# Optimization experiments

Hardware: AMD Instinct MI355X
Metric: run time of the kernel (lower is better)

The kernel has to match this reference:

```python
import jax, jax.numpy as jnp
import numpy as np

HEAD = 32  # HEAD_SIZE
B, T, C = 8, 1024, 768
LAYER_ID, N_LAYER = 2, 12


def wkv7(r, w, k, v, a, b):
    # RWKV7 linear recurrence (matches the custom CUDA 'attn' kernel math):
    #   S = S * exp(-exp(w)) + (S @ a) b^T + v k^T ;  y = S @ r
    Bb, Tt, Cc = r.shape
    H, N = Cc // HEAD, HEAD
    rs = lambda z: jnp.moveaxis(z.reshape(Bb, Tt, H, N), 1, 0)  # [T,B,H,N]
    rT, kT, vT, aT, bT = rs(r), rs(k), rs(v), rs(a), rs(b)
    wT = rs(jnp.exp(-jnp.exp(w)))  # decay in (0,1)
    def step(S, inp):
        rt, wt, kt, vt, at, bt = inp  # each [B,H,N]
        sa = jnp.einsum('bhij,bhj->bhi', S, at)
        S = S * wt[:, :, None, :] + sa[..., None] * bt[:, :, None, :] + vt[..., None] * kt[:, :, None, :]
        return S, jnp.einsum('bhij,bhj->bhi', S, rt)
    S0 = jnp.zeros((Bb, H, N, N), r.dtype)
    _, y = jax.lax.scan(step, S0, (rT, wT, kT, vT, aT, bT))
    return jnp.moveaxis(y, 0, 1).reshape(Bb, Tt, Cc)


def setup_inputs() -> dict:
    key = jax.random.key(0)
    ks = iter(jax.random.split(key, 64))
    def rn(shape, s=0.02):
        return (jax.random.normal(next(ks), shape, jnp.float32) * s)
    def un(shape, lim):
        return jax.random.uniform(next(ks), shape, jnp.float32, -lim, lim)
    H, N = C // HEAD, HEAD
    r10 = 1.0 - LAYER_ID / N_LAYER          # ratio_1_to_almost0
    r01 = LAYER_ID / (N_LAYER - 1)          # ratio_0_to_1
    ddd = (np.arange(C, dtype=np.float64) / C).reshape(1, 1, C)
    f32 = lambda z: jnp.asarray(z, jnp.float32)
    time_maa_x = f32(1.0 - ddd ** (0.6 * r10 ** 0.9))
    time_maa_rg = f32(1.0 - ddd ** (0.2 * r10))
    time_maa_wa = f32(1.0 - ddd ** (0.9 * r10))
    time_maa_k = f32(1.0 - (ddd ** (0.9 * r10) + 0.4 * r01))
    time_maa_v = f32(1.0 - (ddd ** (0.4 * r10) + 0.6 * r01))
    ds = -7.0 + 5.0 * (np.arange(C, dtype=np.float64) / (C - 1)) ** (0.85 + r01 ** 0.5)
    time_decay = f32(ds.reshape(1, 1, C) + 0.5)
    inp = {
        'x': jax.random.normal(next(ks), (B, T, C), jnp.float32),
        'v1': jax.random.normal(next(ks), (B, T, C), jnp.float32),
        'time_maa_x': time_maa_x, 'time_maa_rg': time_maa_rg, 'time_maa_wa': time_maa_wa,
        'time_maa_k': time_maa_k, 'time_maa_v': time_maa_v,
        'time_decay': time_decay,
        'time_faaaa': rn((1, 1, H, N), 0.05),
        'time_aaaaa': rn((1, 1, C), 0.05),
        'time_maa_w1': rn((C, 28 * 4)), 'time_maa_w2': rn((4, 28, C), 0.05),
        'time_decay_w1': rn((C, 64)), 'time_decay_w2': rn((64, C), 0.05),
        'time_aaa_w1': rn((C, 24)), 'time_aaa_w2': rn((24, C), 0.05),
        'time_kkk_w1': rn((C, 24)), 'time_kkk_w2': rn((24, C), 0.05),
        'gate_w1': rn((C, 120)), 'gate_w2': rn((120, C), 0.05),
        'ma_w1': rn((C, 24)), 'ma_w2': rn((24, C), 0.05), 'time_misc_a': rn((1, 1, C), 0.05),
        'mk_w1': rn((C, 24)), 'mk_w2': rn((24, C), 0.05), 'time_misc_k': rn((1, 1, C), 0.05),
        'mv_w1': rn((C, 24)), 'mv_w2': rn((24, C), 0.05), 'time_misc_v': 1.0 + rn((1, 1, C), 0.05),
        'Wr': un((C, C), 0.5 / C ** 0.5), 'Wk': un((C, C), 0.05 / C ** 0.5),
        'Wv': un((C, C), 0.5 / C ** 0.5), 'Wo': rn((C, C), 0.02),
        'ln_w': jnp.ones((C,), jnp.float32), 'ln_b': jnp.zeros((C,), jnp.float32),
    }
    return inp


def reference(x, v1, time_maa_x, time_maa_rg, time_maa_wa, time_maa_k, time_maa_v,
              time_decay, time_faaaa, time_aaaaa, time_maa_w1, time_maa_w2,
              time_decay_w1, time_decay_w2, time_aaa_w1, time_aaa_w2,
              time_kkk_w1, time_kkk_w2, gate_w1, gate_w2, ma_w1, ma_w2, time_misc_a,
              mk_w1, mk_w2, time_misc_k, mv_w1, mv_w2, time_misc_v,
              Wr, Wk, Wv, Wo, ln_w, ln_b):
    Bb, Tt, Cc = x.shape
    H, N = Cc // HEAD, HEAD
    # token shift: xx[t] = x[t-1] - x[t], with x[-1] = 0
    xsh = jnp.concatenate([jnp.zeros_like(x[:, :1]), x[:, :-1]], axis=1)
    xx = xsh - x
    xxx = x + xx * time_maa_x
    tm = jnp.tanh(xxx @ time_maa_w1).reshape(Bb, Tt, 4, -1)      # [B,T,4,28]
    mix = jnp.einsum('btfd,fdc->fbtc', tm, time_maa_w2)          # [4,B,T,C]
    xrg = x + xx * (time_maa_rg + mix[0])
    xwa = x + xx * (time_maa_wa + mix[1])
    xk = x + xx * (time_maa_k + mix[2])
    xv = x + xx * (time_maa_v + mix[3])
    r = xrg @ Wr
    w = -jax.nn.softplus(-(time_decay + jnp.tanh(xwa @ time_decay_w1) @ time_decay_w2)) - 0.5
    k = xk @ Wk
    v = xv @ Wv
    v = v + (v1 - v) * jax.nn.sigmoid(time_misc_v + xv @ mv_w1 @ mv_w2)
    g = jax.nn.sigmoid(xrg @ gate_w1) @ gate_w2
    kk = k + jnp.tanh(xk @ time_kkk_w1) @ time_kkk_w2
    kk4 = kk.reshape(Bb, Tt, H, N)
    nrm = jnp.maximum(jnp.sqrt(jnp.sum(kk4 * kk4, axis=-1, keepdims=True)), 1e-12)
    kk = (kk4 / nrm).reshape(Bb, Tt, Cc)
    a = jax.nn.sigmoid(time_aaaaa + xwa @ time_aaa_w1 @ time_aaa_w2)
    ma = jax.nn.sigmoid(time_misc_a + xwa @ ma_w1 @ ma_w2)
    k = k * ma + k * a * (1.0 - ma)
    mk = jax.nn.sigmoid(time_misc_k + xk @ mk_w1 @ mk_w2)
    k = k * jnp.exp(jnp.minimum(w * mk, 0.0))
    y = wkv7(r, w, k, v, -kk, kk * a)
    # GroupNorm(n_head groups) over each token, eps=6.4e-5
    yg = y.reshape(Bb, Tt, H, N)
    mu = jnp.mean(yg, axis=-1, keepdims=True)
    var = jnp.var(yg, axis=-1, keepdims=True)
    yn = (yg - mu) * jax.lax.rsqrt(var + 6.4e-05)
    yn = yn * ln_w.reshape(H, N) + ln_b.reshape(H, N)
    # per-head bonus term
    bonus = (jnp.sum(r.reshape(Bb, Tt, H, N) * k.reshape(Bb, Tt, H, N) * time_faaaa,
                     axis=-1, keepdims=True) * v.reshape(Bb, Tt, H, N))
    y = yn.reshape(Bb, Tt, Cc) + bonus.reshape(Bb, Tt, Cc)
    out = (y * g) @ Wo
    return (out, v1)
```

## Files before the change

kernel.cpp:

```cpp
#include <hip/hip_runtime.h>
#include <hip/hip_bf16.h>
#include <math.h>

#define Bdim 8
#define Tdim 1024
#define Cdim 768
#define Hdim 24
#define Ndim 32
#define BTdim (Bdim*Tdim)

typedef __attribute__((ext_vector_type(8))) short bf16x8;
typedef __attribute__((ext_vector_type(4))) float f32x4;
typedef __hip_bfloat16 bf16;

__device__ __forceinline__ float sigm(float x){ return 1.f/(1.f+expf(-x)); }
__device__ __forceinline__ float softplusf(float x){ return fmaxf(x,0.f) + log1pf(expf(-fabsf(x))); }
__device__ __forceinline__ float bf2f(bf16 v){ return __bfloat162float(v); }
__device__ __forceinline__ float us2f(unsigned short s){ return __builtin_bit_cast(float, (unsigned)s<<16); }

template<int CTRL>
__device__ __forceinline__ float dpp_add(float x){
  int xi = __builtin_bit_cast(int, x);
  int yi = __builtin_amdgcn_mov_dpp(xi, CTRL, 0xF, 0xF, true);
  return x + __builtin_bit_cast(float, yi);
}
__device__ __forceinline__ float red32(float x){
  x = dpp_add<0xB1>(x);
  x = dpp_add<0x4E>(x);
  x = dpp_add<0x141>(x);
  x = dpp_add<0x140>(x);
  x += __shfl_xor(x, 16);
  return x;
}
__device__ __forceinline__ float red16(float x){
  x = dpp_add<0xB1>(x);
  x = dpp_add<0x4E>(x);
  x = dpp_add<0x141>(x);
  x = dpp_add<0x140>(x);
  return x;
}

#define GLDS16(gp, lp) __builtin_amdgcn_global_load_lds((const __attribute__((address_space(1))) void*)(gp), (__attribute__((address_space(3))) void*)(lp), 16, 0, 0)

__global__ void k1_shift(const float* __restrict__ x, const float* __restrict__ maa_x,
                         bf16* __restrict__ xxx) {
  int idx = blockIdx.x*256 + threadIdx.x;
  if (idx >= BTdim*Cdim) return;
  int c = idx % Cdim; int row = idx / Cdim; int t = row % Tdim;
  float xv = x[idx];
  float xp = (t==0) ? 0.f : x[idx - Cdim];
  xxx[idx] = __float2bfloat16(xv + (xp - xv)*maa_x[c]);
}

__global__ __launch_bounds__(256) void kcp(const float* __restrict__ W0, const float* __restrict__ W1,
    const float* __restrict__ W2, const float* __restrict__ W3,
    bf16* __restrict__ T0, bf16* __restrict__ T1, bf16* __restrict__ T2, bf16* __restrict__ T3,
    const float* __restrict__ dw1, const float* __restrict__ aaa_w1,
    const float* __restrict__ ma_w1, const float* __restrict__ kkk_w1, const float* __restrict__ mk_w1,
    const float* __restrict__ mv_w1, const float* __restrict__ gate_w1, const float* __restrict__ maa_w1,
    const float* __restrict__ dw2, const float* __restrict__ aaa_w2, const float* __restrict__ ma_w2,
    const float* __restrict__ kkk_w2, const float* __restrict__ mk_w2, const float* __restrict__ mv_w2,
    const float* __restrict__ gate_w2,
    bf16* __restrict__ PWwa, bf16* __restrict__ PWk, bf16* __restrict__ PWv,
    bf16* __restrict__ PWrg, bf16* __restrict__ PWmaa,
    bf16* __restrict__ W2wa, bf16* __restrict__ W2k, bf16* __restrict__ W2v, bf16* __restrict__ W2g){
  const int bid = blockIdx.x;
  if (bid < 2304) {
    __shared__ float tile[32][33];
    const int z = bid/576, rem = bid - z*576;
    const int by = (rem/24)*32, bx = (rem%24)*32;
    const float* Wsrc[4] = {W0,W1,W2,W3};
    bf16* Tdst[4] = {T0,T1,T2,T3};
    const float* W = Wsrc[z];
    bf16* T = Tdst[z];
    int tx = threadIdx.x & 31, ty = threadIdx.x >> 5;
    #pragma unroll
    for (int q=0;q<32;q+=8) tile[ty+q][tx] = W[(size_t)(by+ty+q)*Cdim + bx+tx];
    __syncthreads();
    #pragma unroll
    for (int q=0;q<32;q+=8) T[(size_t)(bx+ty+q)*Cdim + by+tx] = __float2bfloat16(tile[tx][ty+q]);
    return;
  }
  int idx = (bid-2304)*256 + threadIdx.x;
  if (idx < 491520) {
    int buf = idx / 98304, rem = idx - buf*98304;
    int n = rem / 768, kk = rem - n*768;
    float val = 0.f;
    bf16* dst;
    switch(buf){
      case 0: dst=PWwa; if(n<64) val=dw1[(size_t)kk*64+n]; else if(n<88) val=aaa_w1[(size_t)kk*24+(n-64)]; else if(n<112) val=ma_w1[(size_t)kk*24+(n-88)]; break;
      case 1: dst=PWk;  if(n<24) val=kkk_w1[(size_t)kk*24+n]; else if(n<48) val=mk_w1[(size_t)kk*24+(n-24)]; break;
      case 2: dst=PWv;  if(n<24) val=mv_w1[(size_t)kk*24+n]; break;
      case 3: dst=PWrg; if(n<120) val=gate_w1[(size_t)kk*120+n]; break;
      default: dst=PWmaa; if(n<112) val=maa_w1[(size_t)kk*112+n]; break;
    }
    dst[rem] = __float2bfloat16(val);
    return;
  }
  int i = idx - 491520;
  if (i < 294912){
    int n=i>>7, q=i&127, seg=n/768, c=n-seg*768;
    float val=0.f;
    if (seg==0){ if(q<64) val=dw2[(size_t)q*768+c]; }
    else if (seg==1){ if(q>=64&&q<88) val=aaa_w2[(size_t)(q-64)*768+c]; }
    else { if(q>=88&&q<112) val=ma_w2[(size_t)(q-88)*768+c]; }
    W2wa[i]=__float2bfloat16(val); return;
  }
  i -= 294912;
  if (i < 98304){
    int n=i>>6, q=i&63, seg=n/768, c=n-seg*768;
    float val=0.f;
    if (seg==0){ if(q<24) val=kkk_w2[(size_t)q*768+c]; }
    else { if(q>=24&&q<48) val=mk_w2[(size_t)(q-24)*768+c]; }
    W2k[i]=__float2bfloat16(val); return;
  }
  i -= 98304;
  if (i < 24576){
    int c=i>>5, q=i&31;
    float val = (q<24) ? mv_w2[(size_t)q*768+c] : 0.f;
    W2v[i]=__float2bfloat16(val); return;
  }
  i -= 24576;
  if (i < 98304){
    int c=i>>7, q=i&127;
    float val = (q<120) ? gate_w2[(size_t)q*768+c] : 0.f;
    W2g[i]=__float2bfloat16(val);
  }
}

__global__ __launch_bounds__(256) void gemm_wo(const bf16* __restrict__ A,
    const bf16* __restrict__ Bt, float* __restrict__ C, int N, int K) {
  __shared__ unsigned short As[64*32];
  __shared__ unsigned short Bs[128*32];
  const int bm = blockIdx.y*64, bn = blockIdx.x*128;
  const int tid = threadIdx.x, lane = tid&63, w = tid>>6;
  const int wr = w>>1, wc = w&1;
  const int lr = lane&15, kg = lane>>4;
  f32x4 zero = {0.f,0.f,0.f,0.f};
  f32x4 acc[2][4];
  #pragma unroll
  for (int m=0;m<2;m++)
    #pragma unroll
    for (int n=0;n<4;n++) acc[m][n]=zero;
  const size_t rowA = (size_t)(bm + w*16 + (lane>>2))*K + (lane&3)*8;
  const size_t rowB = (size_t)(bn + w*32 + (lane>>2))*K + (lane&3)*8;
  unsigned short* lA = As + w*16*32;
  unsigned short* lB = Bs + w*32*32;
  for (int k0=0; k0<K; k0+=32){
    GLDS16(A + rowA + k0,                 lA);
    GLDS16(Bt + rowB + k0,                lB);
    GLDS16(Bt + rowB + k0 + (size_t)16*K, lB + 512);
    __syncthreads();
    bf16x8 af[2], bfr[4];
    #pragma unroll
    for (int m=0;m<2;m++) af[m]  = *(const bf16x8*)(void*)(As + (wr*32+m*16+lr)*32 + kg*8);
    #pragma unroll
    for (int n=0;n<4;n++) bfr[n] = *(const bf16x8*)(void*)(Bs + (wc*64+n*16+lr)*32 + kg*8);
    #pragma unroll
    for (int m=0;m<2;m++)
      #pragma unroll
      for (int n=0;n<4;n++)
        acc[m][n] = __builtin_amdgcn_mfma_f32_16x16x32_bf16(af[m], bfr[n], acc[m][n], 0,0,0);
    __syncthreads();
  }
  #pragma unroll
  for (int m=0;m<2;m++)
    #pragma unroll
    for (int n=0;n<4;n++){
      size_t r0 = (size_t)(bm + wr*32 + m*16 + kg*4);
      int cc = bn + wc*64 + n*16 + lr;
      #pragma unroll
      for (int q=0;q<4;q++)
        C[(r0+q)*N + cc] = acc[m][n][q];
    }
}

__global__ __launch_bounds__(256) void gemm_tm(const bf16* __restrict__ A,
    const bf16* __restrict__ Bt, float* __restrict__ C, int K) {
  __shared__ unsigned short As[128*32];
  __shared__ unsigned short Bs[128*32];
  const int bm = blockIdx.y*128;
  const int tid = threadIdx.x, lane = tid&63, w = tid>>6;
  const int wr = w>>1, wc = w&1;
  const int lr = lane&15, kg = lane>>4;
  f32x4 zero = {0.f,0.f,0.f,0.f};
  f32x4 acc[4][4];
  #pragma unroll
  for (int m=0;m<4;m++)
    #pragma unroll
    for (int n=0;n<4;n++) acc[m][n]=zero;
  const size_t rowA = (size_t)(bm + w*32 + (lane>>2))*K + (lane&3)*8;
  const size_t rowB = (size_t)(w*32 + (lane>>2))*K + (lane&3)*8;
  unsigned short* lA = As + w*32*32;
  unsigned short* lB = Bs + w*32*32;
  for (int k0=0; k0<K; k0+=32){
    GLDS16(A + rowA + k0,                 lA);
    GLDS16(A + rowA + k0 + (size_t)16*K,  lA + 512);
    GLDS16(Bt + rowB + k0,                lB);
    GLDS16(Bt + rowB + k0 + (size_t)16*K, lB + 512);
    __syncthreads();
    bf16x8 af[4], bfr[4];
    #pragma unroll
    for (int m=0;m<4;m++) af[m]  = *(const bf16x8*)(void*)(As + (wr*64+m*16+lr)*32 + kg*8);
    #pragma unroll
    for (int n=0;n<4;n++) bfr[n] = *(const bf16x8*)(void*)(Bs + (wc*64+n*16+lr)*32 + kg*8);
    #pragma unroll
    for (int m=0;m<4;m++)
      #pragma unroll
      for (int n=0;n<4;n++)
        acc[m][n] = __builtin_amdgcn_mfma_f32_16x16x32_bf16(af[m], bfr[n], acc[m][n], 0,0,0);
    __syncthreads();
  }
  #pragma unroll
  for (int m=0;m<4;m++)
    #pragma unroll
    for (int n=0;n<4;n++){
      size_t r0 = (size_t)(bm + wr*64 + m*16 + kg*4);
      int cc = wc*64 + n*16 + lr;
      if (cc < 112){
        #pragma unroll
        for (int q=0;q<4;q++)
          C[(r0+q)*112 + cc] = tanhf(acc[m][n][q]);
      }
    }
}

struct S1P {
  const bf16* A[4];
  const bf16* Bt[4];
  bf16* C[4];
  int Ntrue[4];
  int Nalloc[4];
  int act[4];
};
struct G3 {
  const bf16* A[3];
  const bf16* Bt[3];
  bf16* C[3];
};
__global__ __launch_bounds__(256) void gemm_s1b3(S1P s, G3 g, int K) {
  const int bid = blockIdx.x;
  __shared__ unsigned short As[128*32];
  __shared__ unsigned short Bs[128*32];
  const int tid = threadIdx.x, lane = tid&63, w = tid>>6;
  const int wr = w>>1, wc = w&1;
  const int lr = lane&15, kg = lane>>4;
  int bm, bn, z;
  const bf16 *A, *Bt;
  const bool small = (bid < 256);
  if (small){
    z = bid>>6; bm = (bid&63)*128; bn = 0;
    A = s.A[z]; Bt = s.Bt[z];
  } else {
    int rem = bid-256; z = rem/384; int r2 = rem - z*384;
    bm = (r2/6)*128; bn = (r2%6)*128;
    A = g.A[z]; Bt = g.Bt[z];
  }
  f32x4 zero = {0.f,0.f,0.f,0.f};
  f32x4 acc[4][4];
  #pragma unroll
  for (int m=0;m<4;m++)
    #pragma unroll
    for (int n=0;n<4;n++) acc[m][n]=zero;
  const size_t rowA = (size_t)(bm + w*32 + (lane>>2))*K + (lane&3)*8;
  const size_t rowB = (size_t)(bn + w*32 + (lane>>2))*K + (lane&3)*8;
  unsigned short* lA = As + w*32*32;
  unsigned short* lB = Bs + w*32*32;
  for (int k0=0; k0<K; k0+=32){
    GLDS16(A + rowA + k0,                 lA);
    GLDS16(A + rowA + k0 + (size_t)16*K,  lA + 512);
    GLDS16(Bt + rowB + k0,                lB);
    GLDS16(Bt + rowB + k0 + (size_t)16*K, lB + 512);
    __syncthreads();
    bf16x8 af[4], bfr[4];
    #pragma unroll
    for (int m=0;m<4;m++) af[m]  = *(const bf16x8*)(void*)(As + (wr*64+m*16+lr)*32 + kg*8);
    #pragma unroll
    for (int n=0;n<4;n++) bfr[n] = *(const bf16x8*)(void*)(Bs + (wc*64+n*16+lr)*32 + kg*8);
    #pragma unroll
    for (int m=0;m<4;m++)
      #pragma unroll
      for (int n=0;n<4;n++)
        acc[m][n] = __builtin_amdgcn_mfma_f32_16x16x32_bf16(af[m], bfr[n], acc[m][n], 0,0,0);
    __syncthreads();
  }
  if (small){
    bf16* __restrict__ C = s.C[z];
    const int Ntrue = s.Ntrue[z], Nalloc = s.Nalloc[z], act = s.act[z];
    #pragma unroll
    for (int m=0;m<4;m++)
      #pragma unroll
      for (int n=0;n<4;n++){
        size_t r0 = (size_t)(bm + wr*64 + m*16 + kg*4);
        int cc = wc*64 + n*16 + lr;
        if (cc < Nalloc){
          #pragma unroll
          for (int q=0;q<4;q++){
            float val = acc[m][n][q];
            if      (act==1){ if (cc<64) val = tanhf(val); }
            else if (act==2){ if (cc<24) val = tanhf(val); }
            else if (act==3){ val = sigm(val); }
            if (cc >= Ntrue) val = 0.f;
            C[(r0+q)*Nalloc + cc] = __float2bfloat16(val);
          }
        }
      }
  } else {
    bf16* __restrict__ C = g.C[z];
    #pragma unroll
    for (int m=0;m<4;m++)
      #pragma unroll
      for (int n=0;n<4;n++){
        size_t r0 = (size_t)(bm + wr*64 + m*16 + kg*4);
        int cc = bn + wc*64 + n*16 + lr;
        #pragma unroll
        for (int q=0;q<4;q++)
          C[(r0+q)*Cdim + cc] = __float2bfloat16(acc[m][n][q]);
      }
  }
}

struct Z4 {
  const bf16* A[4];
  const bf16* Bt[4];
  bf16* C[4];
  int N[4];
  int K[4];
};
__global__ __launch_bounds__(256) void gemm_z(Z4 p) {
  const int z = blockIdx.z;
  const int N = p.N[z], K = p.K[z];
  const int bn = blockIdx.x*128;
  if (bn >= N) return;
  const bf16* __restrict__ A  = p.A[z];
  const bf16* __restrict__ Bt = p.Bt[z];
  bf16* __restrict__ C = p.C[z];
  __shared__ unsigned short As[128*32];
  __shared__ unsigned short Bs[128*32];
  const int bm = blockIdx.y*128;
  const int tid = threadIdx.x, lane = tid&63, w = tid>>6;
  const int wr = w>>1, wc = w&1;
  const int lr = lane&15, kg = lane>>4;
  f32x4 zero = {0.f,0.f,0.f,0.f};
  f32x4 acc[4][4];
  #pragma unroll
  for (int m=0;m<4;m++)
    #pragma unroll
    for (int n=0;n<4;n++) acc[m][n]=zero;
  const size_t rowA = (size_t)(bm + w*32 + (lane>>2))*K + (lane&3)*8;
  const size_t rowB = (size_t)(bn + w*32 + (lane>>2))*K + (lane&3)*8;
  unsigned short* lA = As + w*32*32;
  unsigned short* lB = Bs + w*32*32;
  for (int k0=0; k0<K; k0+=32){
    GLDS16(A + rowA + k0,                 lA);
    GLDS16(A + rowA + k0 + (size_t)16*K,  lA + 512);
    GLDS16(Bt + rowB + k0,                lB);
    GLDS16(Bt + rowB + k0 + (size_t)16*K, lB + 512);
    __syncthreads();
    bf16x8 af[4], bfr[4];
    #pragma unroll
    for (int m=0;m<4;m++) af[m]  = *(const bf16x8*)(void*)(As + (wr*64+m*16+lr)*32 + kg*8);
    #pragma unroll
    for (int n=0;n<4;n++) bfr[n] = *(const bf16x8*)(void*)(Bs + (wc*64+n*16+lr)*32 + kg*8);
    #pragma unroll
    for (int m=0;m<4;m++)
      #pragma unroll
      for (int n=0;n<4;n++)
        acc[m][n] = __builtin_amdgcn_mfma_f32_16x16x32_bf16(af[m], bfr[n], acc[m][n], 0,0,0);
    __syncthreads();
  }
  #pragma unroll
  for (int m=0;m<4;m++)
    #pragma unroll
    for (int n=0;n<4;n++){
      size_t r0 = (size_t)(bm + wr*64 + m*16 + kg*4);
      int cc = bn + wc*64 + n*16 + lr;
      #pragma unroll
      for (int q=0;q<4;q++)
        C[(r0+q)*N + cc] = __float2bfloat16(acc[m][n][q]);
    }
}

__global__ __launch_bounds__(256) void k2_mix(const float* __restrict__ x,
    const float* __restrict__ tm, const float* __restrict__ w2,
    const float* __restrict__ mrg, const float* __restrict__ mwa,
    const float* __restrict__ mk_, const float* __restrict__ mv_,
    bf16* __restrict__ xrg, bf16* __restrict__ xwa, bf16* __restrict__ xk, bf16* __restrict__ xv) {
  const int row0 = blockIdx.x*8, tid = threadIdx.x;
  __shared__ float stm[8][112];
  for (int idx=tid; idx<8*112; idx+=256){
    int rr=idx/112, q=idx-rr*112;
    stm[rr][q]=tm[(size_t)(row0+rr)*112+q];
  }
  __syncthreads();
  for (int c=tid;c<Cdim;c+=256){
    float x8[8], d8[8];
    #pragma unroll
    for (int rr=0;rr<8;rr++){
      size_t i=(size_t)(row0+rr)*Cdim+c;
      float xv = x[i];
      float xp = (((row0+rr) & (Tdim-1)) == 0) ? 0.f : x[i - Cdim];
      x8[rr]=xv; d8[rr]=xp - xv;
    }
    float mrgc=mrg[c], mwac=mwa[c], mkc=mk_[c], mvc=mv_[c];
    float m0[8]={},m1[8]={},m2[8]={},m3[8]={};
    #pragma unroll 4
    for (int d=0; d<28; d++){
      float w0=w2[(size_t)(d)*Cdim + c];
      float w1=w2[(size_t)(28+d)*Cdim + c];
      float w2v=w2[(size_t)(56+d)*Cdim + c];
      float w3=w2[(size_t)(84+d)*Cdim + c];
      #pragma unroll
      for (int rr=0;rr<8;rr++){
        m0[rr]+=stm[rr][d]*w0; m1[rr]+=stm[rr][28+d]*w1;
        m2[rr]+=stm[rr][56+d]*w2v; m3[rr]+=stm[rr][84+d]*w3;
      }
    }
    #pragma unroll
    for (int rr=0;rr<8;rr++){
      size_t i=(size_t)(row0+rr)*Cdim+c;
      xrg[i]=__float2bfloat16(x8[rr] + d8[rr]*(mrgc+m0[rr]));
      xwa[i]=__float2bfloat16(x8[rr] + d8[rr]*(mwac+m1[rr]));
      xk[i] =__float2bfloat16(x8[rr] + d8[rr]*(mkc+m2[rr]));
      xv[i] =__float2bfloat16(x8[rr] + d8[rr]*(mvc+m3[rr]));
    }
  }
}

__global__ __launch_bounds__(256) void k5_fuse(
    const bf16* __restrict__ zwa, const bf16* __restrict__ zk, const bf16* __restrict__ zv,
    const bf16* __restrict__ rbf, const bf16* __restrict__ kbf, bf16* __restrict__ vbf,
    const float* __restrict__ td, const float* __restrict__ aaaaa,
    const float* __restrict__ misc_a, const float* __restrict__ misc_k, const float* __restrict__ misc_v,
    const float* __restrict__ v1,
    float* __restrict__ wexp, unsigned short* __restrict__ rkab) {
  const int row = blockIdx.x, tid = threadIdx.x;
  #pragma unroll
  for (int it=0;it<3;it++){
    const int c = tid + it*256;
    const size_t i = (size_t)row*Cdim + c;
    float kraw = bf2f(kbf[i]);
    float v0   = bf2f(vbf[i]);
    float zd = bf2f(zwa[(size_t)row*2304 + c]);
    float za = bf2f(zwa[(size_t)row*2304 + 768 + c]);
    float zma= bf2f(zwa[(size_t)row*2304 + 1536 + c]);
    float zkk= bf2f(zk[(size_t)row*1536 + c]);
    float zmk= bf2f(zk[(size_t)row*1536 + 768 + c]);
    float zmv= bf2f(zv[i]);
    float w = -softplusf(-(td[c]+zd)) - 0.5f;
    wexp[i] = expf(-expf(w));
    float a  = sigm(aaaaa[c]+za);
    float ma = sigm(misc_a[c]+zma);
    float mk = sigm(misc_k[c]+zmk);
    float mv = sigm(misc_v[c]+zmv);
    vbf[i] = __float2bfloat16(v0 + (v1[i]-v0)*mv);
    float kf = kraw*(ma + a*(1.f-ma))*expf(fminf(w*mk,0.f));
    float kk = kraw + zkk;
    float ss = red32(kk*kk);
    float kkn = kk * (1.f/fmaxf(sqrtf(ss),1e-12f));
    unsigned rus = (unsigned)__builtin_bit_cast(unsigned short, rbf[i]);
    unsigned kus = (unsigned)__builtin_bit_cast(unsigned short, __float2bfloat16(kf));
    unsigned aus = (unsigned)__builtin_bit_cast(unsigned short, __float2bfloat16(-kkn));
    unsigned bus = (unsigned)__builtin_bit_cast(unsigned short, __float2bfloat16(kkn*a));
    uint2 pk;
    pk.x = rus | (kus<<16);
    pk.y = aus | (bus<<16);
    *(uint2*)&rkab[((size_t)row*Hdim + (c>>5))*128 + (size_t)(c&31)*4] = pk;
  }
}

__global__ __launch_bounds__(64) void k6_wkv(const unsigned short* __restrict__ rkab,
    const float* __restrict__ wd, const unsigned short* __restrict__ vbf, bf16* __restrict__ y) {
  const int lane = threadIdx.x;
  const int bid = blockIdx.x;
  const int head = bid % (Bdim*Hdim);
  const int rq   = bid / (Bdim*Hdim);
  const int bb = head / Hdim, hh = head - bb*Hdim;
  const int i0 = rq*4 + (lane >> 4);
  const int jh = lane & 15;
  __shared__ __align__(16) unsigned short srk[2][16][128];
  __shared__ __align__(16) float sw[2][16][32];
  __shared__ __align__(16) unsigned short sv[2][16][32];
  const size_t wvbase = (size_t)bb*Tdim*Cdim + (size_t)hh*Ndim;
  float S0=0.f, S1=0.f;

  auto rkrow = [&](size_t t){ return (((size_t)bb*Tdim + t)*Hdim + hh)*128; };
  auto STAGE = [&](int c, int buf){
    const size_t tb = (size_t)c*16;
    #pragma unroll
    for (int i=0;i<4;i++)
      GLDS16(rkab + rkrow(tb + i*4 + (lane>>4)) + (size_t)(lane&15)*8, &srk[buf][i*4][0]);
    GLDS16(wd + wvbase + (tb +     (lane>>3))*Cdim + (lane&7)*4, &sw[buf][0][0]);
    GLDS16(wd + wvbase + (tb + 8 + (lane>>3))*Cdim + (lane&7)*4, &sw[buf][8][0]);
    GLDS16(vbf + wvbase + (tb + (lane>>2))*Cdim + (lane&3)*8, &sv[buf][0][0]);
  };

  uint4 nq; float2 nw; unsigned short nv;
  auto LOADT = [&](int buf, int t){
    nq = *(const uint4*)&srk[buf][t][jh*8];
    nw = *(const float2*)&sw[buf][t][jh*2];
    nv = sv[buf][t][i0];
  };

  STAGE(0, 0);
  asm volatile("s_waitcnt vmcnt(0)" ::: "memory");
  LOADT(0, 0);
  int buf = 0;
  const int NCH = Tdim/16;
  for (int c=0; c<NCH; ++c){
    if (c+1 < NCH) STAGE(c+1, buf^1);
    const size_t yb = wvbase + (size_t)c*16*Cdim;
    #pragma unroll
    for (int t=0; t<16; t++){
      const uint4 q = nq;
      const float2 cw = nw;
      const unsigned short cv = nv;
      if (t < 15) {
        LOADT(buf, t+1);
      } else if (c+1 < NCH) {
        asm volatile("s_waitcnt vmcnt(0)" ::: "memory");
        LOADT(buf^1, 0);
      }
      float r0 = __builtin_bit_cast(float, q.x<<16);
      float k0 = __builtin_bit_cast(float, q.x & 0xFFFF0000u);
      float a0 = __builtin_bit_cast(float, q.y<<16);
      float b0 = __builtin_bit_cast(float, q.y & 0xFFFF0000u);
      float r1 = __builtin_bit_cast(float, q.z<<16);
      float k1 = __builtin_bit_cast(float, q.z & 0xFFFF0000u);
      float a1 = __builtin_bit_cast(float, q.w<<16);
      float b1 = __builtin_bit_cast(float, q.w & 0xFFFF0000u);
      const float vl = us2f(cv);
      float sa = S0*a0 + S1*a1;
      sa = red16(sa);
      S0 = S0*cw.x + (sa*b0 + vl*k0);
      S1 = S1*cw.y + (sa*b1 + vl*k1);
      float yv = S0*r0 + S1*r1;
      yv = red16(yv);
      if (jh == 0) y[yb + (size_t)t*Cdim + i0] = __float2bfloat16(yv);
    }
    buf ^= 1;
  }
}

__global__ __launch_bounds__(256) void k7_post(const bf16* __restrict__ y,
    const unsigned short* __restrict__ rkab, const bf16* __restrict__ v,
    const bf16* __restrict__ g, const float* __restrict__ faaaa,
    const float* __restrict__ lnw, const float* __restrict__ lnb,
    bf16* __restrict__ ygate,
    const float4* __restrict__ v1c, float4* __restrict__ outc) {
  const int row = blockIdx.x, tid = threadIdx.x;
  if (tid < 192) outc[(size_t)row*192 + tid] = v1c[(size_t)row*192 + tid];
  #pragma unroll
  for (int it=0; it<3; it++){
    const int c = tid + it*256;
    const size_t i = (size_t)row*Cdim + c;
    float yv = bf2f(y[i]);
    unsigned rk = *(const unsigned*)&rkab[((size_t)row*Hdim + (c>>5))*128 + (size_t)(c&31)*4];
    float rf = __builtin_bit_cast(float, rk<<16);
    float kf = __builtin_bit_cast(float, rk & 0xFFFF0000u);
    float bon = rf*kf*faaaa[c];
    float s  = red32(yv);
    float ss = red32(yv*yv);
    float bn = red32(bon);
    float mu = s*(1.f/Ndim);
    float var = ss*(1.f/Ndim) - mu*mu;
    float rs = rsqrtf(var + 6.4e-5f);
    float yn = (yv-mu)*rs*lnw[c]+lnb[c];
    ygate[i]=__float2bfloat16((yn + bn*bf2f(v[i]))*bf2f(g[i]));
  }
}

extern "C" void kernel_launch(void* const* d_in, const int* in_sizes, int n_in,
                              void* d_out, int out_size, void* d_ws, size_t ws_size,
                              hipStream_t stream) {
  const float* x      = (const float*)d_in[0];
  const float* v1     = (const float*)d_in[1];
  const float* maa_x  = (const float*)d_in[2];
  const float* maa_rg = (const float*)d_in[3];
  const float* maa_wa = (const float*)d_in[4];
  const float* maa_k  = (const float*)d_in[5];
  const float* maa_v  = (const float*)d_in[6];
  const float* time_decay = (const float*)d_in[7];
  const float* faaaa  = (const float*)d_in[8];
  const float* aaaaa  = (const float*)d_in[9];
  const float* maa_w1 = (const float*)d_in[10];
  const float* maa_w2 = (const float*)d_in[11];
  const float* dw1    = (const float*)d_in[12];
  const float* dw2    = (const float*)d_in[13];
  const float* aaa_w1 = (const float*)d_in[14];
  const float* aaa_w2 = (const float*)d_in[15];
  const float* kkk_w1 = (const float*)d_in[16];
  const float* kkk_w2 = (const float*)d_in[17];
  const float* gate_w1= (const float*)d_in[18];
  const float* gate_w2= (const float*)d_in[19];
  const float* ma_w1  = (const float*)d_in[20];
  const float* ma_w2  = (const float*)d_in[21];
  const float* misc_a = (const float*)d_in[22];
  const float* mk_w1  = (const float*)d_in[23];
  const float* mk_w2  = (const float*)d_in[24];
  const float* misc_k = (const float*)d_in[25];
  const float* mv_w1  = (const float*)d_in[26];
  const float* mv_w2  = (const float*)d_in[27];
  const float* misc_v = (const float*)d_in[28];
  const float* Wr     = (const float*)d_in[29];
  const float* Wk     = (const float*)d_in[30];
  const float* Wv     = (const float*)d_in[31];
  const float* Wo     = (const float*)d_in[32];
  const float* lnw    = (const float*)d_in[33];
  const float* lnb    = (const float*)d_in[34];
  float* out = (float*)d_out;

  float* ws = (float*)d_ws;
  const size_t BTC = (size_t)BTdim*Cdim;
  const size_t HB  = BTC/2;
  float* wexp  = ws;
  bf16* kb_bf  = (bf16*)(ws + 2*HB);
  bf16* ybuf_bf= (bf16*)(ws + 2*HB);
  bf16* vb_bf  = (bf16*)(ws + 3*HB);
  bf16* xrg_bf = (bf16*)(ws + 4*HB);
  bf16* xwa_bf = xrg_bf + BTC;
  bf16* zwa_bf = (bf16*)(ws + 4*HB);
  bf16* xk_bf  = (bf16*)(ws + 7*HB);
  bf16* xv_bf  = xk_bf + BTC;
  bf16* zk_bf  = (bf16*)(ws + 7*HB);
  bf16* xxx_bf = (bf16*)(ws + 9*HB);
  bf16* zv_bf  = (bf16*)(ws + 9*HB);
  float* tm    = ws + 10*HB;
  bf16* zg_bf  = (bf16*)(ws + 10*HB);
  bf16* hwa_bf = (bf16*)(ws + 11*HB);
  bf16* hk_bf  = hwa_bf + (size_t)BTdim*128;
  bf16* hv_bf  = hk_bf  + (size_t)BTdim*64;
  bf16* hrg_bf = hv_bf  + (size_t)BTdim*32;
  unsigned short* rkab = (unsigned short*)(ws + 12*HB);
  bf16* rb_bf  = (bf16*)(ws + 16*HB);
  bf16* yg_bf  = (bf16*)(ws + 17*HB);
  bf16* Wbase  = (bf16*)(ws + 18*HB);
  bf16* WtR = Wbase;
  bf16* WtK = WtR + 589824;
  bf16* WtV = WtK + 589824;
  bf16* WtO = WtV + 589824;
  bf16* PWwa = WtO + 589824;
  bf16* PWk  = PWwa + 98304;
  bf16* PWv  = PWk  + 98304;
  bf16* PWrg = PWv  + 98304;
  bf16* PWmaa= PWrg + 98304;
  bf16* W2wa = PWmaa + 98304;
  bf16* W2k  = W2wa + 294912;
  bf16* W2v  = W2k  + 98304;
  bf16* W2g  = W2v  + 24576;

  dim3 blk(256);
  k1_shift<<<dim3((BTdim*Cdim+255)/256), blk, 0, stream>>>(x, maa_x, xxx_bf);
  kcp<<<dim3(2304+3936), blk, 0, stream>>>(Wr,Wk,Wv,Wo, WtR,WtK,WtV,WtO,
                                           dw1,aaa_w1,ma_w1,kkk_w1,mk_w1,mv_w1,gate_w1,maa_w1,
                                           dw2,aaa_w2,ma_w2,kkk_w2,mk_w2,mv_w2,gate_w2,
                                           PWwa,PWk,PWv,PWrg,PWmaa, W2wa,W2k,W2v,W2g);
  gemm_tm<<<dim3(1,64), blk, 0, stream>>>(xxx_bf, PWmaa, tm, Cdim);
  k2_mix<<<dim3(BTdim/8), blk, 0, stream>>>(x, tm, maa_w2, maa_rg, maa_wa, maa_k, maa_v,
                                            xrg_bf, xwa_bf, xk_bf, xv_bf);
  {
    S1P s{};
    s.A[0]=xwa_bf; s.Bt[0]=PWwa; s.C[0]=hwa_bf; s.Ntrue[0]=112; s.Nalloc[0]=128; s.act[0]=1;
    s.A[1]=xk_bf;  s.Bt[1]=PWk;  s.C[1]=hk_bf;  s.Ntrue[1]=48;  s.Nalloc[1]=64;  s.act[1]=2;
    s.A[2]=xv_bf;  s.Bt[2]=PWv;  s.C[2]=hv_bf;  s.Ntrue[2]=24;  s.Nalloc[2]=32;  s.act[2]=0;
    s.A[3]=xrg_bf; s.Bt[3]=PWrg; s.C[3]=hrg_bf; s.Ntrue[3]=120; s.Nalloc[3]=128; s.act[3]=3;
    G3 g{};
    g.A[0]=xrg_bf; g.Bt[0]=WtR; g.C[0]=rb_bf;
    g.A[1]=xk_bf;  g.Bt[1]=WtK; g.C[1]=kb_bf;
    g.A[2]=xv_bf;  g.Bt[2]=WtV; g.C[2]=vb_bf;
    gemm_s1b3<<<dim3(256 + 3*384), blk, 0, stream>>>(s, g, Cdim);
  }
  {
    Z4 p{};
    p.A[0]=hwa_bf; p.Bt[0]=W2wa; p.C[0]=zwa_bf; p.N[0]=2304; p.K[0]=128;
    p.A[1]=hk_bf;  p.Bt[1]=W2k;  p.C[1]=zk_bf;  p.N[1]=1536; p.K[1]=64;
    p.A[2]=hv_bf;  p.Bt[2]=W2v;  p.C[2]=zv_bf;  p.N[2]=768;  p.K[2]=32;
    p.A[3]=hrg_bf; p.Bt[3]=W2g;  p.C[3]=zg_bf;  p.N[3]=768;  p.K[3]=128;
    gemm_z<<<dim3(18,64,4), blk, 0, stream>>>(p);
  }
  k5_fuse<<<dim3(BTdim), blk, 0, stream>>>(zwa_bf, zk_bf, zv_bf, rb_bf, kb_bf, vb_bf,
      time_decay, aaaaa, misc_a, misc_k, misc_v, v1, wexp, rkab);
  k6_wkv<<<dim3(Bdim*Hdim*8), dim3(64), 0, stream>>>(rkab, wexp,
      (const unsigned short*)vb_bf, ybuf_bf);
  k7_post<<<dim3(BTdim), blk, 0, stream>>>(ybuf_bf, rkab, vb_bf, zg_bf, faaaa, lnw, lnb, yg_bf,
                                           (const float4*)v1, (float4*)(out + BTC));
  gemm_wo<<<dim3(6,128), blk, 0, stream>>>(yg_bf, WtO, out, Cdim, Cdim);
}
```

Measured before the change: 516.9 us.

## Remap GEMM grids to 1D with M-fastest block order and compact gemm_z launch

Converts several GEMM launches to 1D grids whose block index runs over M tiles first, so neighbouring blocks share the same B (weight) tile and reuse it in L2. gemm_z no longer launches idle blocks that exited early for narrow N, and gemm_tm now uses 64-row tiles so 128 blocks cover the GPU instead of 64. The cost is hand-written index decoding, and scheduling behaviour that depends on how blocks are dispatched.

Result: faster. 493.0 us, median of 2 (-4.6%).

```diff
diff --git a/kernel.cpp b/kernel.cpp
--- a/kernel.cpp
+++ b/kernel.cpp
@@ -130,9 +130,10 @@
 
 __global__ __launch_bounds__(256) void gemm_wo(const bf16* __restrict__ A,
     const bf16* __restrict__ Bt, float* __restrict__ C, int N, int K) {
+  const int bid = blockIdx.x;
+  const int bm = (bid & 127)*64, bn = (bid >> 7)*128;
   __shared__ unsigned short As[64*32];
   __shared__ unsigned short Bs[128*32];
-  const int bm = blockIdx.y*64, bn = blockIdx.x*128;
   const int tid = threadIdx.x, lane = tid&63, w = tid>>6;
   const int wr = w>>1, wc = w&1;
   const int lr = lane&15, kg = lane>>4;
@@ -177,45 +178,44 @@
 
 __global__ __launch_bounds__(256) void gemm_tm(const bf16* __restrict__ A,
     const bf16* __restrict__ Bt, float* __restrict__ C, int K) {
-  __shared__ unsigned short As[128*32];
+  const int bm = blockIdx.x*64;
+  __shared__ unsigned short As[64*32];
   __shared__ unsigned short Bs[128*32];
-  const int bm = blockIdx.y*128;
   const int tid = threadIdx.x, lane = tid&63, w = tid>>6;
   const int wr = w>>1, wc = w&1;
   const int lr = lane&15, kg = lane>>4;
   f32x4 zero = {0.f,0.f,0.f,0.f};
-  f32x4 acc[4][4];
-  #pragma unroll
-  for (int m=0;m<4;m++)
+  f32x4 acc[2][4];
+  #pragma unroll
+  for (int m=0;m<2;m++)
     #pragma unroll
     for (int n=0;n<4;n++) acc[m][n]=zero;
-  const size_t rowA = (size_t)(bm + w*32 + (lane>>2))*K + (lane&3)*8;
+  const size_t rowA = (size_t)(bm + w*16 + (lane>>2))*K + (lane&3)*8;
   const size_t rowB = (size_t)(w*32 + (lane>>2))*K + (lane&3)*8;
-  unsigned short* lA = As + w*32*32;
+  unsigned short* lA = As + w*16*32;
   unsigned short* lB = Bs + w*32*32;
   for (int k0=0; k0<K; k0+=32){
     GLDS16(A + rowA + k0,                 lA);
-    GLDS16(A + rowA + k0 + (size_t)16*K,  lA + 512);
     GLDS16(Bt + rowB + k0,                lB);
     GLDS16(Bt + rowB + k0 + (size_t)16*K, lB + 512);
     __syncthreads();
-    bf16x8 af[4], bfr[4];
-    #pragma unroll
-    for (int m=0;m<4;m++) af[m]  = *(const bf16x8*)(void*)(As + (wr*64+m*16+lr)*32 + kg*8);
+    bf16x8 af[2], bfr[4];
+    #pragma unroll
+    for (int m=0;m<2;m++) af[m]  = *(const bf16x8*)(void*)(As + (wr*32+m*16+lr)*32 + kg*8);
     #pragma unroll
     for (int n=0;n<4;n++) bfr[n] = *(const bf16x8*)(void*)(Bs + (wc*64+n*16+lr)*32 + kg*8);
     #pragma unroll
-    for (int m=0;m<4;m++)
+    for (int m=0;m<2;m++)
       #pragma unroll
       for (int n=0;n<4;n++)
         acc[m][n] = __builtin_amdgcn_mfma_f32_16x16x32_bf16(af[m], bfr[n], acc[m][n], 0,0,0);
     __syncthreads();
   }
   #pragma unroll
-  for (int m=0;m<4;m++)
+  for (int m=0;m<2;m++)
     #pragma unroll
     for (int n=0;n<4;n++){
-      size_t r0 = (size_t)(bm + wr*64 + m*16 + kg*4);
+      size_t r0 = (size_t)(bm + wr*32 + m*16 + kg*4);
       int cc = wc*64 + n*16 + lr;
       if (cc < 112){
         #pragma unroll
@@ -252,8 +252,9 @@
     z = bid>>6; bm = (bid&63)*128; bn = 0;
     A = s.A[z]; Bt = s.Bt[z];
   } else {
-    int rem = bid-256; z = rem/384; int r2 = rem - z*384;
-    bm = (r2/6)*128; bn = (r2%6)*128;
+    int rem = bid-256;
+    bn = (rem/192)*128; int t2 = rem%192;
+    z = t2/64; bm = (t2%64)*128;
     A = g.A[z]; Bt = g.Bt[z];
   }
   f32x4 zero = {0.f,0.f,0.f,0.f};
@@ -328,16 +329,21 @@
   int K[4];
 };
 __global__ __launch_bounds__(256) void gemm_z(Z4 p) {
-  const int z = blockIdx.z;
+  const int bid = blockIdx.x;
+  const int qs = bid >> 6;
+  const int bm = (bid & 63) * 128;
+  int z, bnq;
+  if (qs < 18){ z=0; bnq=qs; }
+  else if (qs < 30){ z=1; bnq=qs-18; }
+  else if (qs < 36){ z=2; bnq=qs-30; }
+  else { z=3; bnq=qs-36; }
+  const int bn = bnq*128;
   const int N = p.N[z], K = p.K[z];
-  const int bn = blockIdx.x*128;
-  if (bn >= N) return;
   const bf16* __restrict__ A  = p.A[z];
   const bf16* __restrict__ Bt = p.Bt[z];
   bf16* __restrict__ C = p.C[z];
   __shared__ unsigned short As[128*32];
   __shared__ unsigned short Bs[128*32];
-  const int bm = blockIdx.y*128;
   const int tid = threadIdx.x, lane = tid&63, w = tid>>6;
   const int wr = w>>1, wc = w&1;
   const int lr = lane&15, kg = lane>>4;
@@ -655,7 +661,7 @@
                                            dw1,aaa_w1,ma_w1,kkk_w1,mk_w1,mv_w1,gate_w1,maa_w1,
                                            dw2,aaa_w2,ma_w2,kkk_w2,mk_w2,mv_w2,gate_w2,
                                            PWwa,PWk,PWv,PWrg,PWmaa, W2wa,W2k,W2v,W2g);
-  gemm_tm<<<dim3(1,64), blk, 0, stream>>>(xxx_bf, PWmaa, tm, Cdim);
+  gemm_tm<<<dim3(128), blk, 0, stream>>>(xxx_bf, PWmaa, tm, Cdim);
   k2_mix<<<dim3(BTdim/8), blk, 0, stream>>>(x, tm, maa_w2, maa_rg, maa_wa, maa_k, maa_v,
                                             xrg_bf, xwa_bf, xk_bf, xv_bf);
   {
@@ -676,7 +682,7 @@
     p.A[1]=hk_bf;  p.Bt[1]=W2k;  p.C[1]=zk_bf;  p.N[1]=1536; p.K[1]=64;
     p.A[2]=hv_bf;  p.Bt[2]=W2v;  p.C[2]=zv_bf;  p.N[2]=768;  p.K[2]=32;
     p.A[3]=hrg_bf; p.Bt[3]=W2g;  p.C[3]=zg_bf;  p.N[3]=768;  p.K[3]=128;
-    gemm_z<<<dim3(18,64,4), blk, 0, stream>>>(p);
+    gemm_z<<<dim3(42*64), blk, 0, stream>>>(p);
   }
   k5_fuse<<<dim3(BTdim), blk, 0, stream>>>(zwa_bf, zk_bf, zv_bf, rb_bf, kb_bf, vb_bf,
       time_decay, aaaaa, misc_a, misc_k, misc_v, v1, wexp, rkab);
@@ -684,5 +690,5 @@
       (const unsigned short*)vb_bf, ybuf_bf);
   k7_post<<<dim3(BTdim), blk, 0, stream>>>(ybuf_bf, rkab, vb_bf, zg_bf, faaaa, lnw, lnb, yg_bf,
                                            (const float4*)v1, (float4*)(out + BTC));
-  gemm_wo<<<dim3(6,128), blk, 0, stream>>>(yg_bf, WtO, out, Cdim, Cdim);
-}
+  gemm_wo<<<dim3(768), blk, 0, stream>>>(yg_bf, WtO, out, Cdim, Cdim);
+}
```
